# Kernel tuning notes

Hardware: AMD Instinct MI355X
Metric: run time of the kernel (lower is better)

Reference implementation:

```python
import jax, jax.numpy as jnp
import numpy as np

RECEPTIVE_FIELD = 3  # padding radius r; number of shifts = (2r+1)^2 = 49


def setup_inputs() -> dict:
    key = jax.random.key(0)
    image = jax.random.normal(key, (16, 3, 384, 384), dtype=jnp.float32)
    return {"image": image}


def reference(image):
    r = RECEPTIVE_FIELD
    B, C, H, W = image.shape
    # Pad with +inf, constant mode (torchvision.transforms.Pad(fill=inf))
    padded = jnp.pad(image, ((0, 0), (0, 0), (r, r), (r, r)),
                     mode="constant", constant_values=jnp.inf)
    # Unfold with kernel (H, W) over the padded image enumerates (2r+1)^2
    # shifted HxW windows in row-major (dy, dx) order. For each shift,
    # absolute color distance summed over the 3 channels (cost volume).
    k = 2 * r + 1
    g = jnp.stack(
        [jnp.abs(image - jax.lax.dynamic_slice(padded, (0, 0, dy, dx), (B, C, H, W))).sum(axis=1)
         for dy in range(k) for dx in range(k)],
        axis=1,
    )  # [B, (2r+1)^2, H, W]
    # Original replaces NaNs with inf (inf-padded border artifacts)
    g = jnp.where(jnp.isnan(g), jnp.inf, g)
    return jnp.squeeze(g)
```

## Files before the change

### kernel.cpp

```cpp
#include <hip/hip_runtime.h>
#include <math.h>

#define RF   3
#define KK   7
#define NS   49
#define HH   384
#define WW   384
#define BB   16
#define CC   3
#define TX   64
#define TY   4
#define LX   (TX + 2*RF)
#define LY   (TY + 2*RF)

#define BIG_FINITE 1.0e38f

__global__ __launch_bounds__(TX * TY)
void cost_volume_kernel(const float* __restrict__ img, float* __restrict__ out)
{
    __shared__ float lds[CC][LY][LX];

    const int b      = blockIdx.z;
    const int tile_x = blockIdx.x * TX;
    const int tile_y = blockIdx.y * TY;
    const int tid    = threadIdx.y * TX + threadIdx.x;

    const float INF = __builtin_inff();

    const int total = CC * LY * LX;
    for (int i = tid; i < total; i += TX * TY) {
        int c   = i / (LY * LX);
        int rem = i - c * (LY * LX);
        int ly  = rem / LX;
        int lx  = rem - ly * LX;
        int gy  = tile_y + ly - RF;
        int gx  = tile_x + lx - RF;
        float v = INF;
        if (gy >= 0 && gy < HH && gx >= 0 && gx < WW)
            v = img[(((size_t)b * CC + c) * HH + gy) * WW + gx];
        lds[c][ly][lx] = v;
    }
    __syncthreads();

    const int tx = threadIdx.x, ty = threadIdx.y;
    const float c0 = lds[0][ty + RF][tx + RF];
    const float c1 = lds[1][ty + RF][tx + RF];
    const float c2 = lds[2][ty + RF][tx + RF];

    const int y = tile_y + ty;
    const int x = tile_x + tx;
    float* outp = out + (((size_t)b * NS) * HH + y) * (size_t)WW + x;

    #pragma unroll
    for (int dy = 0; dy < KK; ++dy) {
        #pragma unroll
        for (int dx = 0; dx < KK; ++dx) {
            float g = fabsf(c0 - lds[0][ty + dy][tx + dx])
                    + fabsf(c1 - lds[1][ty + dy][tx + dx])
                    + fabsf(c2 - lds[2][ty + dy][tx + dx]);
            g = fminf(g, BIG_FINITE);
            outp[(size_t)(dy * KK + dx) * HH * WW] = g;
        }
    }
}

extern "C" void kernel_launch(void* const* d_in, const int* in_sizes, int n_in,
                              void* d_out, int out_size, void* d_ws, size_t ws_size,
                              hipStream_t stream)
{
    const float* img = (const float*)d_in[0];
    float* out       = (float*)d_out;

    dim3 grid(WW / TX, HH / TY, BB);
    dim3 block(TX, TY, 1);
    cost_volume_kernel<<<grid, block, 0, stream>>>(img, out);
}
```

Baseline: 110.6 us.

## Register-block 2x4 output pixels per thread with a sliding LDS row window

Each thread now computes a 2-wide by 4-tall block of output pixels instead of one. Neighbor rows are staged from LDS into a four-slot register ring buffer, so each loaded row is reused across the four pixel rows and the seven horizontal shifts. Outputs are written as float2 vector stores, and the grid shrinks to match the larger tiles. The goal is fewer LDS reads and fewer, wider global stores, at the cost of more registers per thread and fewer threads per block.

```diff
diff --git a/kernel.cpp b/kernel.cpp
--- a/kernel.cpp
+++ b/kernel.cpp
@@ -8,27 +8,34 @@
 #define WW   384
 #define BB   16
 #define CC   3
+
 #define TX   64
-#define TY   4
-#define LX   (TX + 2*RF)
-#define LY   (TY + 2*RF)
+#define TY   2
+#define PXW  2
+#define PXH  4
+#define TILE_W (TX*PXW)
+#define TILE_H (TY*PXH)
+#define LX  (TILE_W + 2*RF)
+#define LY  (TILE_H + 2*RF)
 
 #define BIG_FINITE 1.0e38f
 
-__global__ __launch_bounds__(TX * TY)
+__global__ __launch_bounds__(TX*TY)
 void cost_volume_kernel(const float* __restrict__ img, float* __restrict__ out)
 {
     __shared__ float lds[CC][LY][LX];
 
     const int b      = blockIdx.z;
-    const int tile_x = blockIdx.x * TX;
-    const int tile_y = blockIdx.y * TY;
-    const int tid    = threadIdx.y * TX + threadIdx.x;
+    const int tile_x = blockIdx.x * TILE_W;
+    const int tile_y = blockIdx.y * TILE_H;
+    const int tx     = threadIdx.x;
+    const int ty     = threadIdx.y;
+    const int tid    = ty * TX + tx;
 
     const float INF = __builtin_inff();
 
     const int total = CC * LY * LX;
-    for (int i = tid; i < total; i += TX * TY) {
+    for (int i = tid; i < total; i += TX*TY) {
         int c   = i / (LY * LX);
         int rem = i - c * (LY * LX);
         int ly  = rem / LX;
@@ -42,26 +49,63 @@
     }
     __syncthreads();
 
-    const int tx = threadIdx.x, ty = threadIdx.y;
-    const float c0 = lds[0][ty + RF][tx + RF];
-    const float c1 = lds[1][ty + RF][tx + RF];
-    const float c2 = lds[2][ty + RF][tx + RF];
+    float cen[CC][PXH][PXW];
+    #pragma unroll
+    for (int c = 0; c < CC; ++c)
+        #pragma unroll
+        for (int i = 0; i < PXH; ++i)
+            #pragma unroll
+            for (int j = 0; j < PXW; ++j)
+                cen[c][i][j] = lds[c][PXH*ty + i + RF][PXW*tx + RF + j];
 
-    const int y = tile_y + ty;
-    const int x = tile_x + tx;
-    float* outp = out + (((size_t)b * NS) * HH + y) * (size_t)WW + x;
+    float2 w[4][CC][4];
+
+    #define LOAD_ROW(SLOT, RR) do {                                         \
+        _Pragma("unroll")                                                   \
+        for (int c_ = 0; c_ < CC; ++c_) {                                   \
+            const float2* rp_ =                                             \
+                (const float2*)&lds[c_][(RR)][PXW*tx];      \
+            _Pragma("unroll")                                               \
+            for (int k_ = 0; k_ < 4; ++k_) w[(SLOT)][c_][k_] = rp_[k_];     \
+        } } while (0)
+
+    LOAD_ROW(0, PXH*ty + 0);
+    LOAD_ROW(1, PXH*ty + 1);
+    LOAD_ROW(2, PXH*ty + 2);
+
+    const int y0 = tile_y + PXH*ty;
+    const int x0 = tile_x + PXW*tx;
+    float* base = out + ((size_t)b * NS) * (HH*WW) + (size_t)y0 * WW + x0;
 
     #pragma unroll
     for (int dy = 0; dy < KK; ++dy) {
+        LOAD_ROW((dy + 3) & 3, PXH*ty + dy + 3);
         #pragma unroll
         for (int dx = 0; dx < KK; ++dx) {
-            float g = fabsf(c0 - lds[0][ty + dy][tx + dx])
-                    + fabsf(c1 - lds[1][ty + dy][tx + dx])
-                    + fabsf(c2 - lds[2][ty + dy][tx + dx]);
-            g = fminf(g, BIG_FINITE);
-            outp[(size_t)(dy * KK + dx) * HH * WW] = g;
+            float2 res[PXH];
+            #pragma unroll
+            for (int i = 0; i < PXH; ++i) {
+                const int slot = (dy + i) & 3;
+                float g0 = 0.f, g1 = 0.f;
+                #pragma unroll
+                for (int c = 0; c < CC; ++c) {
+                    const float n0 = ((dx + 0) & 1) ? w[slot][c][(dx+0)>>1].y
+                                                    : w[slot][c][(dx+0)>>1].x;
+                    const float n1 = ((dx + 1) & 1) ? w[slot][c][(dx+1)>>1].y
+                                                    : w[slot][c][(dx+1)>>1].x;
+                    g0 += fabsf(cen[c][i][0] - n0);
+                    g1 += fabsf(cen[c][i][1] - n1);
+                }
+                res[i].x = fminf(g0, BIG_FINITE);
+                res[i].y = fminf(g1, BIG_FINITE);
+            }
+            float* sp = base + (size_t)(dy*KK + dx) * (HH*WW);
+            #pragma unroll
+            for (int i = 0; i < PXH; ++i)
+                *(float2*)(sp + (size_t)i * WW) = res[i];
         }
     }
+    #undef LOAD_ROW
 }
 
 extern "C" void kernel_launch(void* const* d_in, const int* in_sizes, int n_in,
@@ -71,7 +115,7 @@
     const float* img = (const float*)d_in[0];
     float* out       = (float*)d_out;
 
-    dim3 grid(WW / TX, HH / TY, BB);
+    dim3 grid(WW / TILE_W, HH / TILE_H, BB);
     dim3 block(TX, TY, 1);
     cost_volume_kernel<<<grid, block, 0, stream>>>(img, out);
 }
```

New measurement: 142.7 us. +29.1%, slower.

## Compute four pixels per thread with vectorized LDS reads and float4 stores

Applied to the files above, without the earlier changes.

Each thread now handles four horizontally adjacent pixels. It loads a 12-wide window row per channel from LDS as float4s and writes the results as float4 stores. This reduces LDS read instructions per output and turns scalar global stores into 16-byte stores, which matters for this write-bound kernel. The LDS row is padded to 136 floats for alignment, at the cost of more registers per thread.

```diff
diff --git a/kernel.cpp b/kernel.cpp
--- a/kernel.cpp
+++ b/kernel.cpp
@@ -8,27 +8,35 @@
 #define WW   384
 #define BB   16
 #define CC   3
-#define TX   64
-#define TY   4
-#define LX   (TX + 2*RF)
-#define LY   (TY + 2*RF)
+#define HW   (HH*WW)
+
+#define TX   32
+#define TY   8
+#define PXW  4
+#define TILE_W (TX*PXW)
+#define TILE_H (TY)
+#define LXR  (TILE_W + 2*RF)
+#define LX   136
+#define LY   (TILE_H + 2*RF)
 
 #define BIG_FINITE 1.0e38f
 
-__global__ __launch_bounds__(TX * TY)
+__global__ __launch_bounds__(TX*TY)
 void cost_volume_kernel(const float* __restrict__ img, float* __restrict__ out)
 {
     __shared__ float lds[CC][LY][LX];
 
     const int b      = blockIdx.z;
-    const int tile_x = blockIdx.x * TX;
-    const int tile_y = blockIdx.y * TY;
-    const int tid    = threadIdx.y * TX + threadIdx.x;
+    const int tile_x = blockIdx.x * TILE_W;
+    const int tile_y = blockIdx.y * TILE_H;
+    const int tx     = threadIdx.x;
+    const int ty     = threadIdx.y;
+    const int tid    = ty * TX + tx;
 
     const float INF = __builtin_inff();
 
     const int total = CC * LY * LX;
-    for (int i = tid; i < total; i += TX * TY) {
+    for (int i = tid; i < total; i += TX*TY) {
         int c   = i / (LY * LX);
         int rem = i - c * (LY * LX);
         int ly  = rem / LX;
@@ -36,30 +44,54 @@
         int gy  = tile_y + ly - RF;
         int gx  = tile_x + lx - RF;
         float v = INF;
-        if (gy >= 0 && gy < HH && gx >= 0 && gx < WW)
+        if (gy >= 0 && gy < HH && gx >= 0 && gx < WW && lx < LXR)
             v = img[(((size_t)b * CC + c) * HH + gy) * WW + gx];
         lds[c][ly][lx] = v;
     }
     __syncthreads();
 
-    const int tx = threadIdx.x, ty = threadIdx.y;
-    const float c0 = lds[0][ty + RF][tx + RF];
-    const float c1 = lds[1][ty + RF][tx + RF];
-    const float c2 = lds[2][ty + RF][tx + RF];
 
-    const int y = tile_y + ty;
-    const int x = tile_x + tx;
-    float* outp = out + (((size_t)b * NS) * HH + y) * (size_t)WW + x;
+    float cen[CC][PXW];
+    {
+        #pragma unroll
+        for (int c = 0; c < CC; ++c) {
+            const float4* rp = (const float4*)&lds[c][ty + RF][PXW*tx];
+            float4 t0 = rp[0], t1 = rp[1];
+            cen[c][0] = t0.w;
+            cen[c][1] = t1.x;
+            cen[c][2] = t1.y;
+            cen[c][3] = t1.z;
+        }
+    }
+
+    const int y0 = tile_y + ty;
+    const int x0 = tile_x + PXW*tx;
+    float* base = out + ((size_t)b * NS) * HW + (size_t)y0 * WW + x0;
 
     #pragma unroll
     for (int dy = 0; dy < KK; ++dy) {
+        float wf[CC][12];
+        #pragma unroll
+        for (int c = 0; c < CC; ++c) {
+            const float4* rp = (const float4*)&lds[c][ty + dy][PXW*tx];
+            float4 t0 = rp[0], t1 = rp[1], t2 = rp[2];
+            wf[c][0]=t0.x; wf[c][1]=t0.y; wf[c][2]=t0.z;  wf[c][3]=t0.w;
+            wf[c][4]=t1.x; wf[c][5]=t1.y; wf[c][6]=t1.z;  wf[c][7]=t1.w;
+            wf[c][8]=t2.x; wf[c][9]=t2.y; wf[c][10]=t2.z; wf[c][11]=t2.w;
+        }
         #pragma unroll
         for (int dx = 0; dx < KK; ++dx) {
-            float g = fabsf(c0 - lds[0][ty + dy][tx + dx])
-                    + fabsf(c1 - lds[1][ty + dy][tx + dx])
-                    + fabsf(c2 - lds[2][ty + dy][tx + dx]);
-            g = fminf(g, BIG_FINITE);
-            outp[(size_t)(dy * KK + dx) * HH * WW] = g;
+            float g[PXW];
+            #pragma unroll
+            for (int j = 0; j < PXW; ++j) {
+                float s = 0.f;
+                #pragma unroll
+                for (int c = 0; c < CC; ++c)
+                    s += fabsf(cen[c][j] - wf[c][dx + j]);
+                g[j] = fminf(s, BIG_FINITE);
+            }
+            float4 res = make_float4(g[0], g[1], g[2], g[3]);
+            *(float4*)(base + (size_t)(dy*KK + dx) * HW) = res;
         }
     }
 }
@@ -71,7 +103,7 @@
     const float* img = (const float*)d_in[0];
     float* out       = (float*)d_out;
 
-    dim3 grid(WW / TX, HH / TY, BB);
+    dim3 grid(WW / TILE_W, HH / TILE_H, BB);
     dim3 block(TX, TY, 1);
     cost_volume_kernel<<<grid, block, 0, stream>>>(img, out);
 }
```

Result: slower. 114.6 us (+3.7%).
